# Optimization experiments

Measured on AMD Instinct MI355X. Metric: run time of the kernel, lower is better.

The kernel has to match this reference:

```python
import jax, jax.numpy as jnp
import numpy as np

SIGMA = 2.0
B, F, N = 4, 64, 4096


def setup_inputs() -> dict:
    key = jax.random.key(0)
    emb_in = jax.random.normal(key, (B, F, N), dtype=jnp.float32)
    adj_in = jnp.zeros((B, N, N), dtype=jnp.float32)  # unused by the module, kept for interface fidelity
    return {"adj_in": adj_in, "emb_in": emb_in}


def reference(adj_in, emb_in):
    # torch .std() is over all elements with Bessel's correction (ddof=1)
    std = jnp.std(emb_in, ddof=1)
    coord = emb_in / std  # [B, F, N]
    fmap = coord.shape[1]
    # mean_f (a-b)^2 = (|a|^2 + |b|^2 - 2 a.b) / F  -- GEMM trick, avoids [B,F,N,N]
    sq = jnp.sum(coord * coord, axis=1)              # [B, N]
    inner = jnp.einsum('bfn,bfm->bnm', coord, coord)  # [B, N, N]
    d2 = (sq[:, :, None] + sq[:, None, :] - 2.0 * inner) / fmap
    d2 = jnp.maximum(d2, 0.0)  # guard tiny negatives from cancellation
    return jnp.exp(-d2 / SIGMA)
```

## Files before the change

kernel.cpp:

```cpp
#include <hip/hip_runtime.h>
#include <hip/hip_bf16.h>

namespace {

constexpr int kB = 4, kF = 64, kN = 4096;
constexpr int kM = kB * kF * kN;

typedef __attribute__((ext_vector_type(8))) short bf16x8;
typedef __attribute__((ext_vector_type(4))) float f32x4;

__device__ __forceinline__ void wave_red2(float& s, float& q) {
#pragma unroll
  for (int o = 32; o > 0; o >>= 1) {
    s += __shfl_down(s, o, 64);
    q += __shfl_down(q, o, 64);
  }
}

__global__ void k_reduce1(const float* __restrict__ emb, float* __restrict__ part) {
  int t = blockIdx.x * blockDim.x + threadIdx.x;
  float4 v = reinterpret_cast<const float4*>(emb)[t];
  float s = v.x + v.y + v.z + v.w;
  float q = v.x * v.x + v.y * v.y + v.z * v.z + v.w * v.w;
  wave_red2(s, q);
  __shared__ float ls[4], lq[4];
  int lane = threadIdx.x & 63, w = threadIdx.x >> 6;
  if (lane == 0) { ls[w] = s; lq[w] = q; }
  __syncthreads();
  if (threadIdx.x == 0) {
    s = ls[0] + ls[1] + ls[2] + ls[3];
    q = lq[0] + lq[1] + lq[2] + lq[3];
    part[blockIdx.x] = s;
    part[1024 + blockIdx.x] = q;
  }
}

__global__ void k_reduce2(float* __restrict__ part) {
  int t = threadIdx.x;
  float s = part[t], q = part[1024 + t];
  wave_red2(s, q);
  __shared__ float ls[16], lq[16];
  int lane = t & 63, w = t >> 6;
  if (lane == 0) { ls[w] = s; lq[w] = q; }
  __syncthreads();
  if (t == 0) {
    s = 0.f; q = 0.f;
#pragma unroll
    for (int i = 0; i < 16; i++) { s += ls[i]; q += lq[i]; }
    float mean = s / (float)kM;
    float var = (q - s * mean) / (float)(kM - 1);
    part[2048] = 1.0f / sqrtf(var);
  }
}

__global__ void k_convert(const float* __restrict__ emb, const float* __restrict__ part,
                          unsigned short* __restrict__ coordT, float* __restrict__ sq) {
  float inv_std = part[2048];
  int g = blockIdx.x * blockDim.x + threadIdx.x;
  int b = g >> 12;
  int n = g & 4095;
  const float* src = emb + ((size_t)b * kF) * kN + n;
  alignas(16) unsigned short loc[kF];
  float acc = 0.f;
#pragma unroll
  for (int f = 0; f < kF; f++) {
    float v = src[(size_t)f * kN] * inv_std;
    union { __hip_bfloat16 h; unsigned short u; } cv;
    cv.h = __float2bfloat16(v);
    loc[f] = cv.u;
    float vf = __bfloat162float(cv.h);
    acc += vf * vf;
  }
  unsigned short* dst = coordT + (size_t)g * kF;
#pragma unroll
  for (int i = 0; i < kF / 8; i++)
    reinterpret_cast<bf16x8*>(dst)[i] = reinterpret_cast<const bf16x8*>(loc)[i];
  sq[g] = acc;
}

__global__ __launch_bounds__(256, 1) void k_gemm_exp(const unsigned short* __restrict__ coordT,
                                                     const float* __restrict__ sq,
                                                     float* __restrict__ out) {
  int b = blockIdx.z;
  int wid = threadIdx.x >> 6;
  int lane = threadIdx.x & 63;
  int lhi = lane >> 4, llo = lane & 15;
  int i0 = blockIdx.y * 128 + (wid >> 1) * 64;
  int j0 = blockIdx.x * 128 + (wid & 1) * 64;
  const unsigned short* base = coordT + (size_t)b * kN * kF;

  bf16x8 af[4][2], bfr[4][2];
#pragma unroll
  for (int m = 0; m < 4; m++) {
    const unsigned short* p = base + (size_t)(i0 + m * 16 + llo) * kF + lhi * 8;
    af[m][0] = *reinterpret_cast<const bf16x8*>(p);
    af[m][1] = *reinterpret_cast<const bf16x8*>(p + 32);
  }
#pragma unroll
  for (int n = 0; n < 4; n++) {
    const unsigned short* p = base + (size_t)(j0 + n * 16 + llo) * kF + lhi * 8;
    bfr[n][0] = *reinterpret_cast<const bf16x8*>(p);
    bfr[n][1] = *reinterpret_cast<const bf16x8*>(p + 32);
  }

  f32x4 acc[4][4] = {};
#pragma unroll
  for (int kk = 0; kk < 2; kk++)
#pragma unroll
    for (int m = 0; m < 4; m++)
#pragma unroll
      for (int n = 0; n < 4; n++)
        acc[m][n] = __builtin_amdgcn_mfma_f32_16x16x32_bf16(af[m][kk], bfr[n][kk], acc[m][n], 0, 0, 0);

  const float* sqb = sq + (size_t)b * kN;
  float si[4][4];
#pragma unroll
  for (int m = 0; m < 4; m++) {
    float4 t = *reinterpret_cast<const float4*>(&sqb[i0 + m * 16 + lhi * 4]);
    si[m][0] = t.x; si[m][1] = t.y; si[m][2] = t.z; si[m][3] = t.w;
  }
  float sj[4];
#pragma unroll
  for (int n = 0; n < 4; n++) sj[n] = sqb[j0 + n * 16 + llo];

  float* ob = out + (size_t)b * kN * kN;
#pragma unroll
  for (int m = 0; m < 4; m++) {
#pragma unroll
    for (int n = 0; n < 4; n++) {
#pragma unroll
      for (int r = 0; r < 4; r++) {
        int i = i0 + m * 16 + lhi * 4 + r;
        int j = j0 + n * 16 + llo;
        float d2 = (si[m][r] + sj[n] - 2.0f * acc[m][n][r]) * (1.0f / 64.0f);
        d2 = fmaxf(d2, 0.0f);
        ob[(size_t)i * kN + j] = __expf(-0.5f * d2);
      }
    }
  }
}

}

extern "C" void kernel_launch(void* const* d_in, const int* in_sizes, int n_in,
                              void* d_out, int out_size, void* d_ws, size_t ws_size,
                              hipStream_t stream) {
  const float* emb = (const float*)d_in[1];
  float* out = (float*)d_out;

  float* part = (float*)d_ws;
  unsigned short* coordT = (unsigned short*)((char*)d_ws + 16384);
  float* sq = (float*)((char*)d_ws + 16384 + (size_t)kB * kN * kF * sizeof(unsigned short));

  k_reduce1<<<1024, 256, 0, stream>>>(emb, part);
  k_reduce2<<<1, 1024, 0, stream>>>(part);
  k_convert<<<(kB * kN) / 256, 256, 0, stream>>>(emb, part, coordT, sq);
  dim3 grid(kN / 128, kN / 128, kB);
  k_gemm_exp<<<grid, 256, 0, stream>>>(coordT, sq, out);
}
```

Baseline: 72.41 us.

## Fuse std finalize into convert, vectorize transposed nontemporal output stores

Drops the single-block reduce2 kernel: every convert block now re-reduces the 1024 partial sums itself, saving one launch. Convert is split four ways across the feature dimension, with a shared-memory reduction of the squared norms, so more threads are in flight. The GEMM epilogue uses the symmetry of the output to write transposed coordinates, giving 16-byte vector stores with a nontemporal hint instead of scalar strided stores. Launch bounds now allow two blocks per CU, at the cost of more register pressure and redundant partial-sum reads per convert block.

```diff
diff --git a/kernel.cpp b/kernel.cpp
--- a/kernel.cpp
+++ b/kernel.cpp
@@ -35,35 +35,37 @@
   }
 }
 
-__global__ void k_reduce2(float* __restrict__ part) {
+__global__ __launch_bounds__(256) void k_convert(const float* __restrict__ emb,
+                                                 const float* __restrict__ part,
+                                                 unsigned short* __restrict__ coordT,
+                                                 float* __restrict__ sq) {
   int t = threadIdx.x;
-  float s = part[t], q = part[1024 + t];
+  float s = part[t] + part[t + 256] + part[t + 512] + part[t + 768];
+  float q = part[1024 + t] + part[1280 + t] + part[1536 + t] + part[1792 + t];
   wave_red2(s, q);
-  __shared__ float ls[16], lq[16];
+  __shared__ float ls[4], lq[4];
+  __shared__ float s_inv;
   int lane = t & 63, w = t >> 6;
   if (lane == 0) { ls[w] = s; lq[w] = q; }
   __syncthreads();
   if (t == 0) {
-    s = 0.f; q = 0.f;
-#pragma unroll
-    for (int i = 0; i < 16; i++) { s += ls[i]; q += lq[i]; }
+    s = ls[0] + ls[1] + ls[2] + ls[3];
+    q = lq[0] + lq[1] + lq[2] + lq[3];
     float mean = s / (float)kM;
     float var = (q - s * mean) / (float)(kM - 1);
-    part[2048] = 1.0f / sqrtf(var);
+    s_inv = 1.0f / sqrtf(var);
   }
-}
+  __syncthreads();
+  float inv_std = s_inv;
 
-__global__ void k_convert(const float* __restrict__ emb, const float* __restrict__ part,
-                          unsigned short* __restrict__ coordT, float* __restrict__ sq) {
-  float inv_std = part[2048];
-  int g = blockIdx.x * blockDim.x + threadIdx.x;
-  int b = g >> 12;
-  int n = g & 4095;
-  const float* src = emb + ((size_t)b * kF) * kN + n;
-  alignas(16) unsigned short loc[kF];
+  int nl = t & 63, fq = t >> 6;
+  int g = blockIdx.x * 64 + nl;
+  int b = g >> 12, n = g & 4095;
+  const float* src = emb + ((size_t)b * kF + fq * 16) * kN + n;
+  alignas(16) unsigned short loc[16];
   float acc = 0.f;
 #pragma unroll
-  for (int f = 0; f < kF; f++) {
+  for (int f = 0; f < 16; f++) {
     float v = src[(size_t)f * kN] * inv_std;
     union { __hip_bfloat16 h; unsigned short u; } cv;
     cv.h = __float2bfloat16(v);
@@ -71,14 +73,17 @@
     float vf = __bfloat162float(cv.h);
     acc += vf * vf;
   }
-  unsigned short* dst = coordT + (size_t)g * kF;
-#pragma unroll
-  for (int i = 0; i < kF / 8; i++)
-    reinterpret_cast<bf16x8*>(dst)[i] = reinterpret_cast<const bf16x8*>(loc)[i];
-  sq[g] = acc;
+  bf16x8* dst = reinterpret_cast<bf16x8*>(coordT + (size_t)g * kF + fq * 16);
+  dst[0] = reinterpret_cast<const bf16x8*>(loc)[0];
+  dst[1] = reinterpret_cast<const bf16x8*>(loc)[1];
+
+  __shared__ float pacc[4][64];
+  pacc[fq][nl] = acc;
+  __syncthreads();
+  if (fq == 0) sq[g] = pacc[0][nl] + pacc[1][nl] + pacc[2][nl] + pacc[3][nl];
 }
 
-__global__ __launch_bounds__(256, 1) void k_gemm_exp(const unsigned short* __restrict__ coordT,
+__global__ __launch_bounds__(256, 2) void k_gemm_exp(const unsigned short* __restrict__ coordT,
                                                      const float* __restrict__ sq,
                                                      float* __restrict__ out) {
   int b = blockIdx.z;
@@ -116,8 +121,8 @@
   float si[4][4];
 #pragma unroll
   for (int m = 0; m < 4; m++) {
-    float4 t = *reinterpret_cast<const float4*>(&sqb[i0 + m * 16 + lhi * 4]);
-    si[m][0] = t.x; si[m][1] = t.y; si[m][2] = t.z; si[m][3] = t.w;
+    f32x4 tv = *reinterpret_cast<const f32x4*>(&sqb[i0 + m * 16 + lhi * 4]);
+    si[m][0] = tv[0]; si[m][1] = tv[1]; si[m][2] = tv[2]; si[m][3] = tv[3];
   }
   float sj[4];
 #pragma unroll
@@ -125,17 +130,18 @@
 
   float* ob = out + (size_t)b * kN * kN;
 #pragma unroll
-  for (int m = 0; m < 4; m++) {
+  for (int n = 0; n < 4; n++) {
+    float* rp = ob + (size_t)(j0 + n * 16 + llo) * kN + i0 + (lhi << 2);
 #pragma unroll
-    for (int n = 0; n < 4; n++) {
+    for (int m = 0; m < 4; m++) {
+      f32x4 wv;
 #pragma unroll
       for (int r = 0; r < 4; r++) {
-        int i = i0 + m * 16 + lhi * 4 + r;
-        int j = j0 + n * 16 + llo;
         float d2 = (si[m][r] + sj[n] - 2.0f * acc[m][n][r]) * (1.0f / 64.0f);
         d2 = fmaxf(d2, 0.0f);
-        ob[(size_t)i * kN + j] = __expf(-0.5f * d2);
+        wv[r] = __expf(-0.5f * d2);
       }
+      __builtin_nontemporal_store(wv, reinterpret_cast<f32x4*>(rp + m * 16));
     }
   }
 }
@@ -153,8 +159,7 @@
   float* sq = (float*)((char*)d_ws + 16384 + (size_t)kB * kN * kF * sizeof(unsigned short));
 
   k_reduce1<<<1024, 256, 0, stream>>>(emb, part);
-  k_reduce2<<<1, 1024, 0, stream>>>(part);
-  k_convert<<<(kB * kN) / 256, 256, 0, stream>>>(emb, part, coordT, sq);
+  k_convert<<<(kB * kN) / 64, 256, 0, stream>>>(emb, part, coordT, sq);
   dim3 grid(kN / 128, kN / 128, kB);
   k_gemm_exp<<<grid, 256, 0, stream>>>(coordT, sq, out);
 }
```

New measurement: 99.08 us. +36.8%, slower.
